# Kernel tuning notes

Measured on AMD Instinct MI355X. Metric: run time of the kernel, lower is better.

## Reference

```python
import jax, jax.numpy as jnp
import numpy as np

B, T, IN_DIM = 64, 256, 256
HID, OUT_DIM = 512, 256
N_LAYERS, N_EXPERTS, N_SHARED = 2, 16, 1


def setup_inputs() -> dict:
    key = jax.random.key(0)
    ks = jax.random.split(key, 10)
    s = 0.02
    x = jax.random.normal(ks[0], (B, T, IN_DIM), dtype=jnp.float32)
    route_id = jax.random.randint(ks[1], (B,), 0, N_EXPERTS)
    Wi = jax.random.normal(ks[2], (HID, IN_DIM), dtype=jnp.float32) * s
    bi = jnp.zeros((HID,), dtype=jnp.float32)
    Wr = jax.random.normal(ks[3], (N_LAYERS, N_EXPERTS, HID, HID), dtype=jnp.float32) * s
    br = jax.random.normal(ks[4], (N_LAYERS, N_EXPERTS, HID), dtype=jnp.float32) * s
    Ws = jax.random.normal(ks[5], (N_LAYERS, N_SHARED, HID, HID), dtype=jnp.float32) * s
    bs = jax.random.normal(ks[6], (N_LAYERS, N_SHARED, HID), dtype=jnp.float32) * s
    Wo = jax.random.normal(ks[7], (OUT_DIM, HID), dtype=jnp.float32) * s
    bo = jnp.zeros((OUT_DIM,), dtype=jnp.float32)
    return {"x": x, "route_id": route_id, "Wi": Wi, "bi": bi, "Wr": Wr,
            "br": br, "Ws": Ws, "bs": bs, "Wo": Wo, "bo": bo}


def reference(x, route_id, Wi, bi, Wr, br, Ws, bs, Wo, bo):
    # flatten tokens: [B, T, in_dim] -> [N, in_dim]
    flat = x.reshape(-1, x.shape[-1])
    n_tok = flat.shape[0]
    # expand route_id: one expert id per batch element -> per token
    route = jnp.repeat(route_id, n_tok // route_id.shape[0])  # [N]
    # projector_i: Linear + ReLU (in_dim != hidden_dim path)
    h = jax.nn.relu(flat @ Wi.T + bi)  # [N, HID]
    n_layers, n_experts = Wr.shape[0], Wr.shape[1]
    for l in range(n_layers):
        # shared experts: mean of per-expert Linear outputs
        shared = (jnp.einsum('nd,shd->snh', h, Ws[l]) + bs[l][:, None, :]).mean(axis=0)
        # routed experts: top_k=1 clustering route -> each token goes to
        # exactly route[token] with weight 1.0 (grouped GEMM, loop over
        # fixed small expert set, masked combine)
        routed = jnp.zeros_like(h)
        for e in range(n_experts):
            ye = h @ Wr[l, e].T + br[l, e]  # [N, HID]
            routed = routed + jnp.where((route == e)[:, None], ye, 0.0)
        h = jax.nn.relu(shared + routed + h)
    out = h @ Wo.T + bo  # [N, OUT_DIM]
    return out.reshape(*x.shape[:-1], out.shape[-1])
```

## Files before the change

### kernel.cpp

```cpp
#include <hip/hip_runtime.h>
#include <hip/hip_bf16.h>
#include <stdint.h>


typedef __attribute__((ext_vector_type(8))) short bf16x8;
typedef __attribute__((ext_vector_type(4))) float f32x4;

#define HPAD 520
#define VMWAIT(N) asm volatile("s_waitcnt vmcnt(" #N ")" ::: "memory")

static __device__ __forceinline__ uint16_t f2bf(float f) {
  union { float f; uint32_t u; } c; c.f = f;
  uint32_t r = (c.u + 0x7FFFu + ((c.u >> 16) & 1u)) >> 16;
  return (uint16_t)r;
}
static __device__ __forceinline__ float bf2f(uint16_t h) {
  union { uint32_t u; float f; } c; c.u = ((uint32_t)h) << 16;
  return c.f;
}

static __device__ __forceinline__ void glds16(const uint16_t* g, uint16_t* l) {
  __builtin_amdgcn_global_load_lds(
      (const __attribute__((address_space(1))) uint32_t*)g,
      (__attribute__((address_space(3))) uint32_t*)l, 16, 0, 0);
}

__global__ __launch_bounds__(256) void k_prep(
    const float* __restrict__ Ws, const float* __restrict__ Wr,
    const float* __restrict__ Wi, const float* __restrict__ Wo,
    const float* __restrict__ bs, const float* __restrict__ br,
    uint16_t* __restrict__ Wcb, uint16_t* __restrict__ Wib,
    uint16_t* __restrict__ Wob, float* __restrict__ bc) {
  int bid = blockIdx.x, tid = threadIdx.x;
  if (bid < 8192) {
    int i = bid * 256 + tid;
    int idx = i * 4;
    int l = idx >> 22;
    int within = idx & (262144 - 1);
    float4 a = *(const float4*)(Ws + l * 262144 + within);
    float4 b = *(const float4*)(Wr + idx);
    ushort4 o;
    o.x = f2bf(a.x + b.x); o.y = f2bf(a.y + b.y);
    o.z = f2bf(a.z + b.z); o.w = f2bf(a.w + b.w);
    ((ushort4*)Wcb)[i] = o;
  } else if (bid < 8320) {
    int i = (bid - 8192) * 256 + tid;
    float4 v = ((const float4*)Wi)[i];
    ushort4 o;
    o.x = f2bf(v.x); o.y = f2bf(v.y); o.z = f2bf(v.z); o.w = f2bf(v.w);
    ((ushort4*)Wib)[i] = o;
  } else if (bid < 8448) {
    int i = (bid - 8320) * 256 + tid;
    float4 v = ((const float4*)Wo)[i];
    ushort4 o;
    o.x = f2bf(v.x); o.y = f2bf(v.y); o.z = f2bf(v.z); o.w = f2bf(v.w);
    ((ushort4*)Wob)[i] = o;
  } else {
    int i = (bid - 8448) * 256 + tid;
    int l = i >> 13, j = i & 511;
    bc[i] = bs[l * 512 + j] + br[i];
  }
}

template <int NT, int KK, int RESID, int F32OUT>
static __device__ __forceinline__ void gemm_phase(
    const uint16_t* __restrict__ W, const float* __restrict__ bias,
    uint16_t* h, float* __restrict__ gout, uint16_t* lS) {
  constexpr int NSTEP = KK / 32;
  constexpr int NC = NT / 8;
  constexpr int NFRAG = NC / 16;
  constexpr int LPS = NFRAG;

  const int tid = threadIdx.x;
  const int lane = tid & 63, wave = tid >> 6;
  const int lr = lane & 15, c0 = lane >> 4;

  uint16_t* lw = lS + wave * 4096;

  const int srow = lane >> 2;
  const int sch = (lane & 3) ^ ((lane >> 3) & 3);
  const uint16_t* wbase = W + (size_t)(wave * NC + srow) * KK + sch * 8;

  auto stage = [&](int buf, int t) {
    #pragma unroll
    for (int j = 0; j < LPS; j++)
      glds16(wbase + (size_t)j * 16 * KK + t * 32,
             lw + buf * (NC * 32) + j * 512);
  };

  const int rb = c0 * 4;
  f32x4 acc[4][NFRAG];
  stage(0, 0);
  stage(1, 1);
  #pragma unroll
  for (int n = 0; n < NFRAG; n++) {
    const int col = wave * NC + n * 16 + lr;
    const float bv = bias[col];
    #pragma unroll
    for (int m = 0; m < 4; m++)
      #pragma unroll
      for (int r = 0; r < 4; r++) {
        float v = bv;
        if constexpr (RESID)
          v += bf2f(h[(size_t)(m * 16 + rb + r) * HPAD + col]);
        acc[m][n][r] = v;
      }
  }

  const int bch = c0 ^ ((lr >> 1) & 3);
  const uint16_t* pB0 = lw + lr * 32 + bch * 8;
  const uint16_t* pA0 = h + (size_t)lr * HPAD + c0 * 8;

  bf16x8 a[2][4], b[2][NFRAG];

  if constexpr (LPS == 4) { VMWAIT(4); } else { VMWAIT(2); }
  #pragma unroll
  for (int m = 0; m < 4; m++)
    a[0][m] = *(const bf16x8*)(pA0 + (size_t)m * 16 * HPAD);
  #pragma unroll
  for (int n = 0; n < NFRAG; n++)
    b[0][n] = *(const bf16x8*)(pB0 + n * 512);

  #pragma unroll
  for (int t = 0; t < NSTEP; t++) {
    const int pp = t & 1;
    if (t + 2 < NSTEP) stage(pp, t + 2);
    if (t + 1 < NSTEP) {
      if (t + 2 < NSTEP) {
        if constexpr (LPS == 4) { VMWAIT(4); } else { VMWAIT(2); }
      } else {
        VMWAIT(0);
      }
      const uint16_t* pBn = pB0 + ((t + 1) & 1) * (NC * 32);
      #pragma unroll
      for (int m = 0; m < 4; m++)
        a[pp ^ 1][m] =
            *(const bf16x8*)(pA0 + (size_t)m * 16 * HPAD + (t + 1) * 32);
      #pragma unroll
      for (int n = 0; n < NFRAG; n++)
        b[pp ^ 1][n] = *(const bf16x8*)(pBn + n * 512);
    }
    #pragma unroll
    for (int m = 0; m < 4; m++)
      #pragma unroll
      for (int n = 0; n < NFRAG; n++)
        acc[m][n] = __builtin_amdgcn_mfma_f32_16x16x32_bf16(
            a[pp][m], b[pp][n], acc[m][n], 0, 0, 0);
  }

  if constexpr (F32OUT) {
    #pragma unroll
    for (int n = 0; n < NFRAG; n++) {
      const int col = wave * NC + n * 16 + lr;
      #pragma unroll
      for (int m = 0; m < 4; m++)
        #pragma unroll
        for (int r = 0; r < 4; r++)
          gout[(size_t)(m * 16 + rb + r) * 256 + col] = acc[m][n][r];
    }
  } else {
    __syncthreads();
    #pragma unroll
    for (int n = 0; n < NFRAG; n++) {
      const int col = wave * NC + n * 16 + lr;
      #pragma unroll
      for (int m = 0; m < 4; m++)
        #pragma unroll
        for (int r = 0; r < 4; r++)
          h[(size_t)(m * 16 + rb + r) * HPAD + col] =
              f2bf(fmaxf(acc[m][n][r], 0.0f));
    }
    __syncthreads();
  }
}

__global__ __launch_bounds__(512) void k_fused(
    const float* __restrict__ x, const int* __restrict__ route,
    const uint16_t* __restrict__ Wib, const float* __restrict__ bi,
    const uint16_t* __restrict__ Wcb, const float* __restrict__ bcb,
    const uint16_t* __restrict__ Wob, const float* __restrict__ bo,
    float* __restrict__ out) {
  __shared__ uint16_t h[64 * HPAD];
  __shared__ uint16_t lS[8 * 4096];

  const int tid = threadIdx.x;
  const int bid = blockIdx.x;
  const int r = bid & 7, q = bid >> 3;
  const int batch = (q >> 2) * 8 + r;
  const int bx = batch * 4 + (q & 3);
  const int e = route[batch];

  const float* gx = x + (size_t)bx * 16384;
  #pragma unroll
  for (int j = 0; j < 8; j++) {
    int fi = j * 2048 + tid * 4;
    float4 v = *(const float4*)(gx + fi);
    int row = fi >> 8, c = fi & 255;
    ushort4 o;
    o.x = f2bf(v.x); o.y = f2bf(v.y); o.z = f2bf(v.z); o.w = f2bf(v.w);
    *(ushort4*)(h + (size_t)row * HPAD + c) = o;
  }
  __syncthreads();

  gemm_phase<512, 256, 0, 0>(Wib, bi, h, nullptr, lS);
  gemm_phase<512, 512, 1, 0>(Wcb + (size_t)e * 262144, bcb + e * 512,
                             h, nullptr, lS);
  gemm_phase<512, 512, 1, 0>(Wcb + (size_t)(16 + e) * 262144,
                             bcb + (16 + e) * 512, h, nullptr, lS);
  gemm_phase<256, 512, 0, 1>(Wob, bo, h, out + (size_t)bx * 16384, lS);
}

extern "C" void kernel_launch(void* const* d_in, const int* in_sizes, int n_in,
                              void* d_out, int out_size, void* d_ws, size_t ws_size,
                              hipStream_t stream) {
  const float* x     = (const float*)d_in[0];
  const int*   route = (const int*)d_in[1];
  const float* Wi    = (const float*)d_in[2];
  const float* bi    = (const float*)d_in[3];
  const float* Wr    = (const float*)d_in[4];
  const float* br    = (const float*)d_in[5];
  const float* Ws    = (const float*)d_in[6];
  const float* bs    = (const float*)d_in[7];
  const float* Wo    = (const float*)d_in[8];
  const float* bo    = (const float*)d_in[9];

  char* ws = (char*)d_ws;
  uint16_t* Wib = (uint16_t*)(ws);
  uint16_t* Wcb = (uint16_t*)(ws + 262144);
  uint16_t* Wob = (uint16_t*)(ws + 17039360);
  float*    bc  = (float*)   (ws + 17301504);

  k_prep<<<8512, 256, 0, stream>>>(Ws, Wr, Wi, Wo, bs, br,
                                   Wcb, Wib, Wob, bc);
  k_fused<<<256, 512, 0, stream>>>(x, route, Wib, bi, Wcb, bc, Wob, bo,
                                   (float*)d_out);
}
```

Measured before the change: 50.24 us.

## Load weight fragments directly to registers and halve token tile per block

Drops the LDS staging of weight tiles through global_load_lds and has each lane load its B fragments straight from global memory into registers, double-buffered. The block shrinks to 32 tokens and 4 waves, each wave covering a quarter of the output columns, and the grid doubles to 512 blocks with two blocks allowed per CU. This removes the LDS round trip and its shared-memory footprint and raises parallelism, at the cost of reading each weight element from global memory twice as often across blocks and possibly worse memory coalescing.

```diff
diff --git a/kernel.cpp b/kernel.cpp
--- a/kernel.cpp
+++ b/kernel.cpp
@@ -17,12 +17,6 @@
 static __device__ __forceinline__ float bf2f(uint16_t h) {
   union { uint32_t u; float f; } c; c.u = ((uint32_t)h) << 16;
   return c.f;
-}
-
-static __device__ __forceinline__ void glds16(const uint16_t* g, uint16_t* l) {
-  __builtin_amdgcn_global_load_lds(
-      (const __attribute__((address_space(1))) uint32_t*)g,
-      (__attribute__((address_space(3))) uint32_t*)l, 16, 0, 0);
 }
 
 __global__ __launch_bounds__(256) void k_prep(
@@ -65,39 +59,33 @@
 template <int NT, int KK, int RESID, int F32OUT>
 static __device__ __forceinline__ void gemm_phase(
     const uint16_t* __restrict__ W, const float* __restrict__ bias,
-    uint16_t* h, float* __restrict__ gout, uint16_t* lS) {
+    uint16_t* h, float* __restrict__ gout) {
   constexpr int NSTEP = KK / 32;
-  constexpr int NC = NT / 8;
+  constexpr int NC = NT / 4;
   constexpr int NFRAG = NC / 16;
-  constexpr int LPS = NFRAG;
 
   const int tid = threadIdx.x;
   const int lane = tid & 63, wave = tid >> 6;
   const int lr = lane & 15, c0 = lane >> 4;
-
-  uint16_t* lw = lS + wave * 4096;
-
-  const int srow = lane >> 2;
-  const int sch = (lane & 3) ^ ((lane >> 3) & 3);
-  const uint16_t* wbase = W + (size_t)(wave * NC + srow) * KK + sch * 8;
-
-  auto stage = [&](int buf, int t) {
-    #pragma unroll
-    for (int j = 0; j < LPS; j++)
-      glds16(wbase + (size_t)j * 16 * KK + t * 32,
-             lw + buf * (NC * 32) + j * 512);
-  };
-
   const int rb = c0 * 4;
-  f32x4 acc[4][NFRAG];
-  stage(0, 0);
-  stage(1, 1);
+
+  const uint16_t* wb = W + (size_t)(wave * NC + lr) * KK + c0 * 8;
+
+  bf16x8 b[2][NFRAG];
+  #pragma unroll
+  for (int n = 0; n < NFRAG; n++)
+    b[0][n] = *(const bf16x8*)(wb + (size_t)n * 16 * KK);
+  #pragma unroll
+  for (int n = 0; n < NFRAG; n++)
+    b[1][n] = *(const bf16x8*)(wb + (size_t)n * 16 * KK + 32);
+
+  f32x4 acc[2][NFRAG];
   #pragma unroll
   for (int n = 0; n < NFRAG; n++) {
     const int col = wave * NC + n * 16 + lr;
     const float bv = bias[col];
     #pragma unroll
-    for (int m = 0; m < 4; m++)
+    for (int m = 0; m < 2; m++)
       #pragma unroll
       for (int r = 0; r < 4; r++) {
         float v = bv;
@@ -107,45 +95,37 @@
       }
   }
 
-  const int bch = c0 ^ ((lr >> 1) & 3);
-  const uint16_t* pB0 = lw + lr * 32 + bch * 8;
   const uint16_t* pA0 = h + (size_t)lr * HPAD + c0 * 8;
-
-  bf16x8 a[2][4], b[2][NFRAG];
-
-  if constexpr (LPS == 4) { VMWAIT(4); } else { VMWAIT(2); }
-  #pragma unroll
-  for (int m = 0; m < 4; m++)
+  bf16x8 a[2][2];
+  #pragma unroll
+  for (int m = 0; m < 2; m++)
     a[0][m] = *(const bf16x8*)(pA0 + (size_t)m * 16 * HPAD);
-  #pragma unroll
-  for (int n = 0; n < NFRAG; n++)
-    b[0][n] = *(const bf16x8*)(pB0 + n * 512);
 
   #pragma unroll
   for (int t = 0; t < NSTEP; t++) {
     const int pp = t & 1;
-    if (t + 2 < NSTEP) stage(pp, t + 2);
     if (t + 1 < NSTEP) {
-      if (t + 2 < NSTEP) {
-        if constexpr (LPS == 4) { VMWAIT(4); } else { VMWAIT(2); }
-      } else {
-        VMWAIT(0);
-      }
-      const uint16_t* pBn = pB0 + ((t + 1) & 1) * (NC * 32);
-      #pragma unroll
-      for (int m = 0; m < 4; m++)
+      if constexpr (NFRAG == 8) { VMWAIT(8); } else { VMWAIT(4); }
+    } else {
+      VMWAIT(0);
+    }
+    if (t + 1 < NSTEP) {
+      #pragma unroll
+      for (int m = 0; m < 2; m++)
         a[pp ^ 1][m] =
             *(const bf16x8*)(pA0 + (size_t)m * 16 * HPAD + (t + 1) * 32);
-      #pragma unroll
-      for (int n = 0; n < NFRAG; n++)
-        b[pp ^ 1][n] = *(const bf16x8*)(pBn + n * 512);
-    }
-    #pragma unroll
-    for (int m = 0; m < 4; m++)
+    }
+    #pragma unroll
+    for (int m = 0; m < 2; m++)
       #pragma unroll
       for (int n = 0; n < NFRAG; n++)
         acc[m][n] = __builtin_amdgcn_mfma_f32_16x16x32_bf16(
             a[pp][m], b[pp][n], acc[m][n], 0, 0, 0);
+    if (t + 2 < NSTEP) {
+      #pragma unroll
+      for (int n = 0; n < NFRAG; n++)
+        b[pp][n] = *(const bf16x8*)(wb + (size_t)n * 16 * KK + (t + 2) * 32);
+    }
   }
 
   if constexpr (F32OUT) {
@@ -153,7 +133,7 @@
     for (int n = 0; n < NFRAG; n++) {
       const int col = wave * NC + n * 16 + lr;
       #pragma unroll
-      for (int m = 0; m < 4; m++)
+      for (int m = 0; m < 2; m++)
         #pragma unroll
         for (int r = 0; r < 4; r++)
           gout[(size_t)(m * 16 + rb + r) * 256 + col] = acc[m][n][r];
@@ -164,7 +144,7 @@
     for (int n = 0; n < NFRAG; n++) {
       const int col = wave * NC + n * 16 + lr;
       #pragma unroll
-      for (int m = 0; m < 4; m++)
+      for (int m = 0; m < 2; m++)
         #pragma unroll
         for (int r = 0; r < 4; r++)
           h[(size_t)(m * 16 + rb + r) * HPAD + col] =
@@ -174,26 +154,25 @@
   }
 }
 
-__global__ __launch_bounds__(512) void k_fused(
+__global__ __launch_bounds__(256, 2) void k_fused(
     const float* __restrict__ x, const int* __restrict__ route,
     const uint16_t* __restrict__ Wib, const float* __restrict__ bi,
     const uint16_t* __restrict__ Wcb, const float* __restrict__ bcb,
     const uint16_t* __restrict__ Wob, const float* __restrict__ bo,
     float* __restrict__ out) {
-  __shared__ uint16_t h[64 * HPAD];
-  __shared__ uint16_t lS[8 * 4096];
+  __shared__ uint16_t h[32 * HPAD];
 
   const int tid = threadIdx.x;
   const int bid = blockIdx.x;
   const int r = bid & 7, q = bid >> 3;
-  const int batch = (q >> 2) * 8 + r;
-  const int bx = batch * 4 + (q & 3);
+  const int batch = (q >> 3) * 8 + r;
+  const int bx = batch * 8 + (q & 7);
   const int e = route[batch];
 
-  const float* gx = x + (size_t)bx * 16384;
+  const float* gx = x + (size_t)bx * 8192;
   #pragma unroll
   for (int j = 0; j < 8; j++) {
-    int fi = j * 2048 + tid * 4;
+    int fi = j * 1024 + tid * 4;
     float4 v = *(const float4*)(gx + fi);
     int row = fi >> 8, c = fi & 255;
     ushort4 o;
@@ -202,12 +181,12 @@
   }
   __syncthreads();
 
-  gemm_phase<512, 256, 0, 0>(Wib, bi, h, nullptr, lS);
+  gemm_phase<512, 256, 0, 0>(Wib, bi, h, nullptr);
   gemm_phase<512, 512, 1, 0>(Wcb + (size_t)e * 262144, bcb + e * 512,
-                             h, nullptr, lS);
+                             h, nullptr);
   gemm_phase<512, 512, 1, 0>(Wcb + (size_t)(16 + e) * 262144,
-                             bcb + (16 + e) * 512, h, nullptr, lS);
-  gemm_phase<256, 512, 0, 1>(Wob, bo, h, out + (size_t)bx * 16384, lS);
+                             bcb + (16 + e) * 512, h, nullptr);
+  gemm_phase<256, 512, 0, 1>(Wob, bo, h, out + (size_t)bx * 8192);
 }
 
 extern "C" void kernel_launch(void* const* d_in, const int* in_sizes, int n_in,
@@ -232,6 +211,6 @@
 
   k_prep<<<8512, 256, 0, stream>>>(Ws, Wr, Wi, Wo, bs, br,
                                    Wcb, Wib, Wob, bc);
-  k_fused<<<256, 512, 0, stream>>>(x, route, Wib, bi, Wcb, bc, Wob, bo,
+  k_fused<<<512, 256, 0, stream>>>(x, route, Wib, bi, Wcb, bc, Wob, bo,
                                    (float*)d_out);
 }
```

Result: slower. 104.9 us (+108.7%).
